# Performance work log

Measured on AMD Instinct MI355X. Metric: run time of the kernel, lower is better.

## Reference

```python
import jax, jax.numpy as jnp
import numpy as np

N_POINTS = 1 << 20
N_LEVELS = 16
F_PER_LVL = 2
LOG2_T = 19
T = 1 << LOG2_T
BASE_RES = 16
PER_LEVEL_SCALE = float(np.exp2(np.log2(2048.0 / 16.0) / (N_LEVELS - 1)))
# 8 trilinear corner offsets [8,3]
OFFSETS = np.stack(np.meshgrid(*([np.array([0, 1])] * 3), indexing='ij'), axis=-1).reshape(8, 3)
PRIMES = np.array([1, 2654435761, 805459861], dtype=np.uint32)  # tcnn spatial hash primes


def _level_params(l):
    # tcnn: grid_scale = 2^(l*log2(s)) * base - 1 ; resolution = ceil(scale)+1
    scale = np.exp2(l * np.log2(PER_LEVEL_SCALE)) * BASE_RES - 1.0
    res = int(np.ceil(scale)) + 1
    return float(scale), res


def hash_encode(x, table):
    """x: [N,3] in [0,1]; table: [L,T,F]. Returns [N, L*F]."""
    offs = jnp.asarray(OFFSETS)                     # [8,3] int32
    primes = jnp.asarray(PRIMES)                    # [3] uint32
    feats = []
    for l in range(N_LEVELS):
        scale, res = _level_params(l)
        pos = x * scale + 0.5                       # [N,3]
        pos_grid = jnp.floor(pos)
        w = pos - pos_grid                          # [N,3] interp weights
        c0 = pos_grid.astype(jnp.int32)             # [N,3]
        corners = c0[None, :, :] + offs[:, None, :]  # [8,N,3]
        if res ** 3 <= T:
            # dense indexing for coarse levels (fits in hashmap)
            cc = jnp.clip(corners, 0, res - 1)
            idx = cc[..., 0] + cc[..., 1] * res + cc[..., 2] * (res * res)
        else:
            cu = corners.astype(jnp.uint32)
            h = (cu[..., 0] * primes[0]) ^ (cu[..., 1] * primes[1]) ^ (cu[..., 2] * primes[2])
            idx = (h & jnp.uint32(T - 1)).astype(jnp.int32)
        f = table[l][idx]                           # [8,N,F] gather
        # trilinear weights: prod over dims of (w if corner bit else 1-w)
        wc = jnp.prod(jnp.where(offs[:, None, :] == 1, w[None], 1.0 - w[None]), axis=-1)  # [8,N]
        feats.append(jnp.sum(wc[..., None] * f, axis=0))  # [N,F]
    return jnp.concatenate(feats, axis=-1)          # [N, 32]


def _softplus10(z):
    return jax.nn.softplus(10.0 * z) / 10.0


def setup_inputs() -> dict:
    key = jax.random.key(0)
    k = jax.random.split(key, 6)
    x = jax.random.uniform(k[0], (N_POINTS, 3), dtype=jnp.float32)
    table = jax.random.normal(k[1], (N_LEVELS, T, F_PER_LVL), dtype=jnp.float32) * 1e-2
    w1 = jax.random.normal(k[2], (64, 32), dtype=jnp.float32) * 0.1
    w2 = jax.random.normal(k[3], (64, 64), dtype=jnp.float32) * 0.1
    w3 = jax.random.normal(k[4], (64, 64), dtype=jnp.float32) * 0.1
    w4 = jax.random.normal(k[5], (1, 64), dtype=jnp.float32) * 0.1
    return {"x": x, "table": table, "w1": w1, "w2": w2, "w3": w3, "w4": w4}


def reference(x, table, w1, w2, w3, w4):
    enc = hash_encode(x, table)                     # [N,32]
    h = _softplus10(enc @ w1.T)
    h = _softplus10(h @ w2.T)
    h = _softplus10(h @ w3.T)
    sdf = h @ w4.T                                  # [N,1]
    return sdf
```

## Files before the change

### kernel.cpp

```cpp
#include <hip/hip_runtime.h>
#include <cmath>

#define T_SIZE (1u << 19)
#define CB 512
#define NBLK 512
#define RCAP 3584

typedef _Float16 h8 __attribute__((ext_vector_type(8)));
typedef _Float16 h4 __attribute__((ext_vector_type(4)));
typedef _Float16 h2 __attribute__((ext_vector_type(2)));
typedef float f4 __attribute__((ext_vector_type(4)));

struct Levels {
    float scale[16];
    int   res[16];
    unsigned dense_mask;
};

__device__ __forceinline__ float softplus10(float z) {
    float e = __builtin_amdgcn_exp2f(fminf(z * 14.426950408889634f, 126.0f));
    return __builtin_amdgcn_logf(1.0f + e) * 0.069314718055994531f;
}

__device__ __forceinline__ unsigned spread3(unsigned v) {
    v &= 1023u;
    v = (v | (v << 16)) & 0x030000FFu;
    v = (v | (v << 8))  & 0x0300F00Fu;
    v = (v | (v << 4))  & 0x030C30C3u;
    v = (v | (v << 2))  & 0x09249249u;
    return v;
}

__device__ __forceinline__ unsigned morton_key(float px, float py, float pz) {
    unsigned qx = (unsigned)fminf(fmaxf(px, 0.f) * 32.f, 31.f);
    unsigned qy = (unsigned)fminf(fmaxf(py, 0.f) * 32.f, 31.f);
    unsigned qz = (unsigned)fminf(fmaxf(pz, 0.f) * 32.f, 31.f);
    return (spread3(qx) << 2) | (spread3(qy) << 1) | spread3(qz);
}

__global__ __launch_bounds__(256) void convert_kernel(
    const float2* __restrict__ t, h2* __restrict__ o, int total4,
    const float* __restrict__ w1, const float* __restrict__ w2,
    const float* __restrict__ w3, _Float16* __restrict__ wh,
    const float* __restrict__ xs, unsigned short* __restrict__ M, int N)
{
    const int histStart = (total4 + 10240 + 255) >> 8;
    if ((int)blockIdx.x >= histStart) {
        __shared__ unsigned h[CB];
        const int blk = blockIdx.x - histStart;
        for (int t2 = threadIdx.x; t2 < CB; t2 += 256) h[t2] = 0u;
        __syncthreads();
        const int s = blk * 2048;
#pragma unroll
        for (int j = 0; j < 8; ++j) {
            int i = s + threadIdx.x + j * 256;
            unsigned k = morton_key(xs[3 * i], xs[3 * i + 1], xs[3 * i + 2]) >> 6;
            atomicAdd(&h[k], 1u);
        }
        __syncthreads();
        for (int t2 = threadIdx.x; t2 < CB; t2 += 256)
            M[t2 * NBLK + blk] = (unsigned short)h[t2];
        return;
    }
    int i = blockIdx.x * 256 + threadIdx.x;
    if (i < total4) {
        const float2* src = t + (size_t)i * 4;
        h8 r;
#pragma unroll
        for (int j = 0; j < 4; ++j) {
            float2 v = src[j];
            r[2 * j]     = (_Float16)v.x;
            r[2 * j + 1] = (_Float16)v.y;
        }
        *(h8*)(o + (size_t)i * 4) = r;
    } else {
        int k = i - total4;
        if (k < 10240) {
            float v = (k < 2048) ? w1[k] : (k < 6144) ? w2[k - 2048] : w3[k - 6144];
            wh[k] = (_Float16)v;
        }
    }
}

__global__ __launch_bounds__(1024) void scan_kernel(
    const unsigned short* __restrict__ M, unsigned* __restrict__ Ms)
{
    __shared__ unsigned tmp[1024];
    const int t = threadIdx.x;
    const int PERS = (CB * NBLK) / 1024;
    unsigned s = 0;
    for (int j = 0; j < PERS; ++j) s += M[t * PERS + j];
    tmp[t] = s;
    __syncthreads();
    for (int d = 1; d < 1024; d <<= 1) {
        unsigned v = (t >= d) ? tmp[t - d] : 0u;
        __syncthreads();
        tmp[t] += v;
        __syncthreads();
    }
    unsigned run = (t > 0) ? tmp[t - 1] : 0u;
    for (int j = 0; j < PERS; ++j) {
        unsigned v = M[t * PERS + j];
        Ms[t * PERS + j] = run;
        run += v;
    }
}

__global__ __launch_bounds__(256) void cscatter_kernel(
    const float* __restrict__ xs, const unsigned* __restrict__ Ms,
    float4* __restrict__ sx4, int N)
{
    __shared__ float4  pts[2048];
    __shared__ unsigned gp[2048];
    __shared__ unsigned lh[CB];
    __shared__ unsigned lbase[CB];
    __shared__ unsigned tmp[256];
    const int tid = threadIdx.x;
    const int blk = blockIdx.x;
    for (int t2 = tid; t2 < CB; t2 += 256) lh[t2] = 0u;
    __syncthreads();
    const int s = blk * 2048;
    float4  myp[8];
    unsigned myk[8];
#pragma unroll
    for (int j = 0; j < 8; ++j) {
        int i = s + tid + j * 256;
        float px = xs[3 * i], py = xs[3 * i + 1], pz = xs[3 * i + 2];
        myp[j] = make_float4(px, py, pz, __uint_as_float((unsigned)i));
        myk[j] = morton_key(px, py, pz) >> 6;
        atomicAdd(&lh[myk[j]], 1u);
    }
    __syncthreads();
    unsigned a0 = lh[2 * tid], a1 = lh[2 * tid + 1];
    tmp[tid] = a0 + a1;
    __syncthreads();
    for (int d = 1; d < 256; d <<= 1) {
        unsigned v = (tid >= d) ? tmp[tid - d] : 0u;
        __syncthreads();
        tmp[tid] += v;
        __syncthreads();
    }
    unsigned eb = (tid > 0) ? tmp[tid - 1] : 0u;
    lbase[2 * tid] = eb;
    lbase[2 * tid + 1] = eb + a0;
    __syncthreads();
    lh[2 * tid] = 0u; lh[2 * tid + 1] = 0u;
    __syncthreads();
#pragma unroll
    for (int j = 0; j < 8; ++j) {
        unsigned k = myk[j];
        unsigned r = atomicAdd(&lh[k], 1u);
        unsigned slot = lbase[k] + r;
        pts[slot] = myp[j];
        gp[slot] = Ms[k * NBLK + blk] + r;
    }
    __syncthreads();
    for (int j = tid; j < 2048; j += 256)
        sx4[gp[j]] = pts[j];
}

__global__ __launch_bounds__(256) void refine_kernel(
    float4* __restrict__ sx4, const unsigned* __restrict__ Ms, int N)
{
    __shared__ float4 pts[RCAP];
    __shared__ unsigned h[64], base[64];
    const int b = blockIdx.x;
    const unsigned s = Ms[b * NBLK];
    const unsigned e = (b == CB - 1) ? (unsigned)N : Ms[(b + 1) * NBLK];
    const unsigned cnt = e - s;
    if (cnt > RCAP) return;
    if (threadIdx.x < 64) h[threadIdx.x] = 0u;
    __syncthreads();
    for (unsigned i = threadIdx.x; i < cnt; i += 256) {
        float4 q = sx4[s + i];
        pts[i] = q;
        unsigned k = morton_key(q.x, q.y, q.z) & 63u;
        atomicAdd(&h[k], 1u);
    }
    __syncthreads();
    if (threadIdx.x == 0) {
        unsigned a = 0;
        for (int j = 0; j < 64; ++j) { base[j] = a; a += h[j]; }
    }
    __syncthreads();
    if (threadIdx.x < 64) h[threadIdx.x] = 0u;
    __syncthreads();
    for (unsigned i = threadIdx.x; i < cnt; i += 256) {
        float4 q = pts[i];
        unsigned k = morton_key(q.x, q.y, q.z) & 63u;
        unsigned r = base[k] + atomicAdd(&h[k], 1u);
        sx4[s + r] = q;
    }
}

__device__ __forceinline__ void gather_pair(
    const h2* __restrict__ tl, unsigned i0, unsigned i1,
    float2& v0, float2& v1)
{
    unsigned e0, e1;
    if ((i0 ^ i1) == 1u) {
        uint2 both = *(const uint2*)(tl + (i0 & ~1u));
        e0 = (i0 & 1u) ? both.y : both.x;
        e1 = (i0 & 1u) ? both.x : both.y;
    } else {
        e0 = *(const unsigned*)(tl + i0);
        e1 = *(const unsigned*)(tl + i1);
    }
    h2 c0 = __builtin_bit_cast(h2, e0);
    h2 c1 = __builtin_bit_cast(h2, e1);
    v0 = make_float2((float)c0[0], (float)c0[1]);
    v1 = make_float2((float)c1[0], (float)c1[1]);
}

__device__ __forceinline__ h2 encode_point(
    float px, float py, float pz, float s, int res, bool dense,
    const h2* __restrict__ tl)
{
    float fx = px * s + 0.5f, fy = py * s + 0.5f, fz = pz * s + 0.5f;
    float gx = floorf(fx), gy = floorf(fy), gz = floorf(fz);
    float wx = fx - gx, wy = fy - gy, wz = fz - gz;
    int cx = (int)gx, cy = (int)gy, cz = (int)gz;

    float2 vx0[4], vx1[4];
    if (dense) {
        int r1 = res - 1;
        int x0 = min(cx, r1), x1 = min(cx + 1, r1);
        int y0 = min(cy, r1), y1 = min(cy + 1, r1);
        int z0 = min(cz, r1), z1 = min(cz + 1, r1);
        int rr = res * res;
        int bases[4] = {y0 * res + z0 * rr, y0 * res + z1 * rr,
                        y1 * res + z0 * rr, y1 * res + z1 * rr};
#pragma unroll
        for (int j = 0; j < 4; ++j)
            gather_pair(tl, (unsigned)(x0 + bases[j]), (unsigned)(x1 + bases[j]),
                        vx0[j], vx1[j]);
    } else {
        unsigned hy0 = (unsigned)cy * 2654435761u, hy1 = (unsigned)(cy + 1) * 2654435761u;
        unsigned hz0 = (unsigned)cz * 805459861u,  hz1 = (unsigned)(cz + 1) * 805459861u;
        unsigned Y[4] = {hy0 ^ hz0, hy0 ^ hz1, hy1 ^ hz0, hy1 ^ hz1};
        const unsigned M = T_SIZE - 1;
#pragma unroll
        for (int j = 0; j < 4; ++j)
            gather_pair(tl, ((unsigned)cx ^ Y[j]) & M,
                        ((unsigned)(cx + 1) ^ Y[j]) & M, vx0[j], vx1[j]);
    }

    float wx0 = 1.f - wx, wy0 = 1.f - wy, wz0 = 1.f - wz;
    float wyz[4] = {wy0 * wz0, wy0 * wz, wy * wz0, wy * wz};
    float f0 = 0.f, f1 = 0.f;
#pragma unroll
    for (int j = 0; j < 4; ++j) {
        float w0 = wx0 * wyz[j], w1 = wx * wyz[j];
        f0 += w0 * vx0[j].x + w1 * vx1[j].x;
        f1 += w0 * vx0[j].y + w1 * vx1[j].y;
    }
    h2 r; r[0] = (_Float16)f0; r[1] = (_Float16)f1;
    return r;
}

__global__ __launch_bounds__(256) void encode_kernel(
    const float* __restrict__ xs, const h2* __restrict__ table,
    h2* __restrict__ enc2, Levels lv, int lbase, int N)
{
    __shared__ float sx[768];
    const int i0 = blockIdx.x * 256;
    for (int t = threadIdx.x; t < 768; t += 256) sx[t] = xs[(size_t)i0 * 3 + t];
    __syncthreads();

    const int l = lbase + blockIdx.y;
    const int i = i0 + threadIdx.x;
    if (i >= N) return;
    h2 r = encode_point(sx[threadIdx.x * 3], sx[threadIdx.x * 3 + 1],
                        sx[threadIdx.x * 3 + 2], lv.scale[l], lv.res[l],
                        (lv.dense_mask >> l) & 1u, table + (size_t)l * T_SIZE);
    enc2[(size_t)l * N + i] = r;
}

__global__ __launch_bounds__(256) void encode_kernel_sorted(
    const float4* __restrict__ xs4, const h2* __restrict__ table,
    h2* __restrict__ enc2, Levels lv, int lbase, int N)
{
    const int i = blockIdx.x * 256 + threadIdx.x;
    if (i >= N) return;
    const int l = lbase + blockIdx.y;
    float4 q = xs4[i];
    h2 r = encode_point(q.x, q.y, q.z, lv.scale[l], lv.res[l],
                        (lv.dense_mask >> l) & 1u, table + (size_t)l * T_SIZE);
    enc2[(size_t)l * N + i] = r;
}

template <typename WT>
__device__ __forceinline__ h8 load_frag8(const WT* p) {
    if constexpr (sizeof(WT) == 2) {
        return *(const h8*)p;
    } else {
        h8 r;
#pragma unroll
        for (int j = 0; j < 8; ++j) r[j] = (_Float16)p[j];
        return r;
    }
}

template <typename WT, bool LOCAL, bool SORTED>
__global__ __launch_bounds__(256, 3) void fused_kernel(
    const float* __restrict__ xs, const float4* __restrict__ xs4,
    const h2* __restrict__ table16, const h2* __restrict__ enc2,
    const WT* __restrict__ w1, const WT* __restrict__ w2,
    const WT* __restrict__ w3, const float* __restrict__ w4,
    float* __restrict__ out, Levels lv, int N)
{
    constexpr int AR = 72;
    __shared__ __align__(16) char smem[4 * 9216];
    __shared__ float sx[768];

    const int tid  = threadIdx.x;
    const int wave = tid >> 6;
    const int lane = tid & 63;
    const int lrow = lane & 15;
    const int quad = lane >> 4;
    const int base = blockIdx.x * 256;
    char* wmem = smem + wave * 9216;
    const f4 zero = {0.f, 0.f, 0.f, 0.f};

    float px, py, pz;
    unsigned oi = 0;
    if constexpr (SORTED) {
        float4 q = xs4[base + tid];
        px = q.x; py = q.y; pz = q.z;
        oi = __float_as_uint(q.w);
    } else {
        for (int t = tid; t < 768; t += 256) sx[t] = xs[(size_t)base * 3 + t];
        __syncthreads();
        px = sx[tid * 3]; py = sx[tid * 3 + 1]; pz = sx[tid * 3 + 2];
    }
    const int p = tid & 63;

    if (LOCAL) {
#pragma unroll
        for (int l = 5; l < 15; ++l) {
            h2 v = enc2[(size_t)l * N + base + tid];
            *(h2*)(wmem + ((l >> 2) << 10) + (p << 4) + ((l & 3) << 2)) = v;
        }
        const int LMAP[6] = {0, 1, 2, 3, 4, 15};
#pragma unroll 2
        for (int s6 = 0; s6 < 6; ++s6) {
            const int l = LMAP[s6];
            h2 v = encode_point(px, py, pz, lv.scale[l], lv.res[l],
                                (lv.dense_mask >> l) & 1u,
                                table16 + (size_t)l * T_SIZE);
            *(h2*)(wmem + ((l >> 2) << 10) + (p << 4) + ((l & 3) << 2)) = v;
        }
    } else {
#pragma unroll
        for (int l = 0; l < 16; ++l) {
            h2 v = enc2[(size_t)l * N + base + tid];
            *(h2*)(wmem + ((l >> 2) << 10) + (p << 4) + ((l & 3) << 2)) = v;
        }
    }

    asm volatile("" ::: "memory");

    h8 aW1[4];
#pragma unroll
    for (int tm = 0; tm < 4; ++tm)
        aW1[tm] = load_frag8(w1 + (tm * 16 + lrow) * 32 + quad * 8);
    h8 aW2[4][2], aW3[4][2];
#pragma unroll
    for (int tm = 0; tm < 4; ++tm)
#pragma unroll
        for (int km = 0; km < 2; ++km) {
            aW2[tm][km] = load_frag8(w2 + (tm * 16 + lrow) * 64 + km * 32 + quad * 8);
            aW3[tm][km] = load_frag8(w3 + (tm * 16 + lrow) * 64 + km * 32 + quad * 8);
        }
    h4 w4q[4];
#pragma unroll
    for (int tm = 0; tm < 4; ++tm)
#pragma unroll
        for (int r = 0; r < 4; ++r) w4q[tm][r] = (_Float16)w4[tm * 16 + quad * 4 + r];

    h8 bin[4];
#pragma unroll
    for (int t = 0; t < 4; ++t)
        bin[t] = *(const h8*)(wmem + (quad << 10) + ((t * 16 + lrow) << 4));

    _Float16* wAct = (_Float16*)wmem;

#pragma unroll
    for (int t = 0; t < 4; ++t) {
        const int arow = (t * 16 + lrow) * AR;
#pragma unroll
        for (int tm = 0; tm < 4; ++tm) {
            f4 acc = __builtin_amdgcn_mfma_f32_16x16x32_f16(aW1[tm], bin[t], zero, 0, 0, 0);
            h4 pk;
#pragma unroll
            for (int r = 0; r < 4; ++r) pk[r] = (_Float16)softplus10(acc[r]);
            *(h4*)&wAct[arow + tm * 16 + quad * 4] = pk;
        }
    }

#pragma unroll
    for (int t = 0; t < 4; ++t) {
        const int arow = (t * 16 + lrow) * AR;
        h8 b0 = *(const h8*)&wAct[arow + quad * 8];
        h8 b1 = *(const h8*)&wAct[arow + 32 + quad * 8];
        f4 accs[4];
#pragma unroll
        for (int tm = 0; tm < 4; ++tm) {
            f4 acc = __builtin_amdgcn_mfma_f32_16x16x32_f16(aW2[tm][0], b0, zero, 0, 0, 0);
            acc     = __builtin_amdgcn_mfma_f32_16x16x32_f16(aW2[tm][1], b1, acc,  0, 0, 0);
            accs[tm] = acc;
        }
#pragma unroll
        for (int tm = 0; tm < 4; ++tm) {
            h4 pk;
#pragma unroll
            for (int r = 0; r < 4; ++r) pk[r] = (_Float16)softplus10(accs[tm][r]);
            *(h4*)&wAct[arow + tm * 16 + quad * 4] = pk;
        }
    }

#pragma unroll
    for (int t = 0; t < 4; ++t) {
        const int arow = (t * 16 + lrow) * AR;
        h8 b0 = *(const h8*)&wAct[arow + quad * 8];
        h8 b1 = *(const h8*)&wAct[arow + 32 + quad * 8];
        float sum = 0.f;
#pragma unroll
        for (int tm = 0; tm < 4; ++tm) {
            f4 acc = __builtin_amdgcn_mfma_f32_16x16x32_f16(aW3[tm][0], b0, zero, 0, 0, 0);
            acc     = __builtin_amdgcn_mfma_f32_16x16x32_f16(aW3[tm][1], b1, acc,  0, 0, 0);
#pragma unroll
            for (int r = 0; r < 4; ++r)
                sum += (float)w4q[tm][r] * softplus10(acc[r]);
        }
        sum += __shfl_xor(sum, 16, 64);
        sum += __shfl_xor(sum, 32, 64);
        if constexpr (SORTED) {
            unsigned t_oi = __shfl(oi, t * 16 + lrow, 64);
            if (quad == 0) out[t_oi] = sum;
        } else {
            if (quad == 0)
                out[base + wave * 64 + t * 16 + lrow] = sum;
        }
    }
}

__global__ __launch_bounds__(256) void encode_kernel_f32(
    const float* __restrict__ xs, const float2* __restrict__ table,
    h2* __restrict__ enc2, Levels lv, int N)
{
    const int i = blockIdx.x * 256 + threadIdx.x;
    const int l = blockIdx.y;
    if (i >= N) return;
    float px = xs[3 * i], py = xs[3 * i + 1], pz = xs[3 * i + 2];
    float s = lv.scale[l];
    int res = lv.res[l];
    float fx = px * s + 0.5f, fy = py * s + 0.5f, fz = pz * s + 0.5f;
    float gx = floorf(fx), gy = floorf(fy), gz = floorf(fz);
    float wx = fx - gx, wy = fy - gy, wz = fz - gz;
    int cx = (int)gx, cy = (int)gy, cz = (int)gz;
    unsigned idx[8];
    if ((lv.dense_mask >> l) & 1u) {
        int r1 = res - 1;
        int x0 = min(cx, r1), x1 = min(cx + 1, r1);
        int y0 = min(cy, r1), y1 = min(cy + 1, r1);
        int z0 = min(cz, r1), z1 = min(cz + 1, r1);
        int rr = res * res;
        idx[0] = x0 + y0 * res + z0 * rr; idx[1] = x0 + y0 * res + z1 * rr;
        idx[2] = x0 + y1 * res + z0 * rr; idx[3] = x0 + y1 * res + z1 * rr;
        idx[4] = x1 + y0 * res + z0 * rr; idx[5] = x1 + y0 * res + z1 * rr;
        idx[6] = x1 + y1 * res + z0 * rr; idx[7] = x1 + y1 * res + z1 * rr;
    } else {
        unsigned hx0 = (unsigned)cx, hx1 = (unsigned)(cx + 1);
        unsigned hy0 = (unsigned)cy * 2654435761u, hy1 = (unsigned)(cy + 1) * 2654435761u;
        unsigned hz0 = (unsigned)cz * 805459861u,  hz1 = (unsigned)(cz + 1) * 805459861u;
        idx[0] = (hx0^hy0^hz0) & (T_SIZE-1); idx[1] = (hx0^hy0^hz1) & (T_SIZE-1);
        idx[2] = (hx0^hy1^hz0) & (T_SIZE-1); idx[3] = (hx0^hy1^hz1) & (T_SIZE-1);
        idx[4] = (hx1^hy0^hz0) & (T_SIZE-1); idx[5] = (hx1^hy0^hz1) & (T_SIZE-1);
        idx[6] = (hx1^hy1^hz0) & (T_SIZE-1); idx[7] = (hx1^hy1^hz1) & (T_SIZE-1);
    }
    const float2* tl = table + (size_t)l * T_SIZE;
    float wx0 = 1.f - wx, wy0 = 1.f - wy, wz0 = 1.f - wz;
    float wcs[8] = {wx0*wy0*wz0, wx0*wy0*wz, wx0*wy*wz0, wx0*wy*wz,
                    wx*wy0*wz0,  wx*wy0*wz,  wx*wy*wz0,  wx*wy*wz};
    float f0 = 0.f, f1 = 0.f;
#pragma unroll
    for (int c = 0; c < 8; ++c) {
        float2 v = tl[idx[c]];
        f0 += wcs[c] * v.x; f1 += wcs[c] * v.y;
    }
    h2 r; r[0] = (_Float16)f0; r[1] = (_Float16)f1;
    enc2[(size_t)l * N + i] = r;
}

extern "C" void kernel_launch(void* const* d_in, const int* in_sizes, int n_in,
                              void* d_out, int out_size, void* d_ws, size_t ws_size,
                              hipStream_t stream) {
    const float* x     = (const float*)d_in[0];
    const float* table = (const float*)d_in[1];
    const float* w1    = (const float*)d_in[2];
    const float* w2    = (const float*)d_in[3];
    const float* w3    = (const float*)d_in[4];
    const float* w4    = (const float*)d_in[5];
    float* out = (float*)d_out;
    const int N = in_sizes[0] / 3;

    Levels lv;
    lv.dense_mask = 0;
    const double pls = exp2(log2(2048.0 / 16.0) / 15.0);
    const double lg  = log2(pls);
    for (int l = 0; l < 16; ++l) {
        double sc = exp2((double)l * lg) * 16.0 - 1.0;
        int res = (int)ceil(sc) + 1;
        lv.scale[l] = (float)sc;
        lv.res[l]   = res;
        if ((long long)res * res * res <= (long long)T_SIZE) lv.dense_mask |= (1u << l);
    }

    const size_t encBytes   = (size_t)16 * N * 4;
    const size_t tableBytes = (size_t)16 * T_SIZE * 4;
    const size_t whBytes    = 32768;
    const size_t sx4Bytes   = (size_t)N * 16;
    h2* enc2 = (h2*)d_ws;

    const int ptBlocks = (N + 255) / 256;

    if (ws_size >= encBytes + tableBytes + whBytes + sx4Bytes
        && N == NBLK * 2048) {
        h2* table16    = (h2*)((char*)d_ws + encBytes);
        _Float16* wh   = (_Float16*)((char*)d_ws + encBytes + tableBytes);
        float4* sx4    = (float4*)((char*)d_ws + encBytes + tableBytes + whBytes);
        unsigned short* M = (unsigned short*)d_ws;
        unsigned* Ms      = (unsigned*)((char*)d_ws + 1024 * 1024);

        const int total4 = 16 * T_SIZE / 4;
        const int convBlocks = (total4 + 10240 + 255) / 256;
        hipLaunchKernelGGL(convert_kernel, dim3(convBlocks + NBLK), dim3(256), 0,
                           stream, (const float2*)table, table16, total4,
                           w1, w2, w3, wh, x, M, N);
        hipLaunchKernelGGL(scan_kernel, dim3(1), dim3(1024), 0, stream, M, Ms);
        hipLaunchKernelGGL(cscatter_kernel, dim3(NBLK), dim3(256), 0, stream,
                           x, Ms, sx4, N);
        hipLaunchKernelGGL(refine_kernel, dim3(CB), dim3(256), 0, stream,
                           sx4, Ms, N);

        hipLaunchKernelGGL(encode_kernel_sorted, dim3(ptBlocks, 10), dim3(256), 0, stream,
                           (const float4*)sx4, (const h2*)table16, enc2, lv, 5, N);
        hipLaunchKernelGGL((fused_kernel<_Float16, true, true>), dim3(ptBlocks), dim3(256),
                           0, stream, x, (const float4*)sx4, (const h2*)table16,
                           (const h2*)enc2, wh, wh + 2048, wh + 6144, w4, out, lv, N);
    } else if (ws_size >= encBytes + tableBytes + whBytes) {
        h2* table16 = (h2*)((char*)d_ws + encBytes);
        _Float16* wh = (_Float16*)((char*)d_ws + encBytes + tableBytes);
        const int total4 = 16 * T_SIZE / 4;
        const int convBlocks = (total4 + 10240 + 255) / 256;
        hipLaunchKernelGGL(convert_kernel, dim3(convBlocks), dim3(256), 0, stream,
                           (const float2*)table, table16, total4, w1, w2, w3, wh,
                           x, (unsigned short*)nullptr, N);
        hipLaunchKernelGGL(encode_kernel, dim3(ptBlocks, 10), dim3(256), 0, stream,
                           x, (const h2*)table16, enc2, lv, 5, N);
        hipLaunchKernelGGL((fused_kernel<_Float16, true, false>), dim3(ptBlocks), dim3(256),
                           0, stream, x, (const float4*)nullptr, (const h2*)table16,
                           (const h2*)enc2, wh, wh + 2048, wh + 6144, w4, out, lv, N);
    } else {
        hipLaunchKernelGGL(encode_kernel_f32, dim3(ptBlocks, 16), dim3(256), 0, stream,
                           x, (const float2*)table, enc2, lv, N);
        hipLaunchKernelGGL((fused_kernel<float, false, false>), dim3(ptBlocks), dim3(256),
                           0, stream, x, (const float4*)nullptr, (const h2*)nullptr,
                           (const h2*)enc2, w1, w2, w3, w4, out, lv, N);
    }
}
```

Measured before the change: 481.3 us.

## Widen table gathers to 16-byte loads and process two points per thread

The corner gather now loads an aligned 16-byte group of four fp16 feature pairs, so the x-neighbour is taken from the same load whenever both fall in that group. The sorted encode kernel runs two points per thread: it computes all indices first, issues every gather, then interpolates, giving more loads in flight per thread. The scan kernel also reads its histogram with 16-byte vector loads. This adds register pressure and makes each gather wider than before, and the sorted encode kernel drops its bounds check, relying on N being a multiple of 512.

Measured after the change: 475.2 us. About the same (-1.3%).

```diff
diff --git a/kernel.cpp b/kernel.cpp
--- a/kernel.cpp
+++ b/kernel.cpp
@@ -88,8 +88,14 @@
     __shared__ unsigned tmp[1024];
     const int t = threadIdx.x;
     const int PERS = (CB * NBLK) / 1024;
+    const uint4* mv = (const uint4*)(M + t * PERS);
     unsigned s = 0;
-    for (int j = 0; j < PERS; ++j) s += M[t * PERS + j];
+#pragma unroll 4
+    for (int j = 0; j < PERS / 8; ++j) {
+        uint4 v = mv[j];
+        s += (v.x & 0xFFFFu) + (v.x >> 16) + (v.y & 0xFFFFu) + (v.y >> 16)
+           + (v.z & 0xFFFFu) + (v.z >> 16) + (v.w & 0xFFFFu) + (v.w >> 16);
+    }
     tmp[t] = s;
     __syncthreads();
     for (int d = 1; d < 1024; d <<= 1) {
@@ -197,13 +203,20 @@
     const h2* __restrict__ tl, unsigned i0, unsigned i1,
     float2& v0, float2& v1)
 {
-    unsigned e0, e1;
-    if ((i0 ^ i1) == 1u) {
-        uint2 both = *(const uint2*)(tl + (i0 & ~1u));
-        e0 = (i0 & 1u) ? both.y : both.x;
-        e1 = (i0 & 1u) ? both.x : both.y;
-    } else {
-        e0 = *(const unsigned*)(tl + i0);
+    unsigned g = i0 & ~3u;
+    union { h8 v; uint4 u; } cv;
+    cv.v = *(const h8*)(tl + g);
+    unsigned p0 = i0 & 3u;
+    unsigned a01 = (p0 & 1u) ? cv.u.y : cv.u.x;
+    unsigned a23 = (p0 & 1u) ? cv.u.w : cv.u.z;
+    unsigned e0  = (p0 & 2u) ? a23 : a01;
+    unsigned e1;
+    if ((i1 & ~3u) == g) {
+        unsigned p1 = i1 & 3u;
+        unsigned b01 = (p1 & 1u) ? cv.u.y : cv.u.x;
+        unsigned b23 = (p1 & 1u) ? cv.u.w : cv.u.z;
+        e1 = (p1 & 2u) ? b23 : b01;
+    } else {
         e1 = *(const unsigned*)(tl + i1);
     }
     h2 c0 = __builtin_bit_cast(h2, e0);
@@ -258,6 +271,79 @@
     return r;
 }
 
+struct PLCtx {
+    unsigned g[4], p0[4], i1[4], sg[4];
+    float wx, wy, wz;
+};
+
+__device__ __forceinline__ void prep_point(
+    float px, float py, float pz, float s, int res, bool dense, PLCtx& c)
+{
+    float fx = px * s + 0.5f, fy = py * s + 0.5f, fz = pz * s + 0.5f;
+    float gx = floorf(fx), gy = floorf(fy), gz = floorf(fz);
+    c.wx = fx - gx; c.wy = fy - gy; c.wz = fz - gz;
+    int cx = (int)gx, cy = (int)gy, cz = (int)gz;
+    unsigned i0[4], i1[4];
+    if (dense) {
+        int r1 = res - 1;
+        int x0 = min(cx, r1), x1 = min(cx + 1, r1);
+        int y0 = min(cy, r1), y1 = min(cy + 1, r1);
+        int z0 = min(cz, r1), z1 = min(cz + 1, r1);
+        int rr = res * res;
+        int bases[4] = {y0 * res + z0 * rr, y0 * res + z1 * rr,
+                        y1 * res + z0 * rr, y1 * res + z1 * rr};
+#pragma unroll
+        for (int j = 0; j < 4; ++j) {
+            i0[j] = (unsigned)(x0 + bases[j]);
+            i1[j] = (unsigned)(x1 + bases[j]);
+        }
+    } else {
+        unsigned hy0 = (unsigned)cy * 2654435761u, hy1 = (unsigned)(cy + 1) * 2654435761u;
+        unsigned hz0 = (unsigned)cz * 805459861u,  hz1 = (unsigned)(cz + 1) * 805459861u;
+        unsigned Y[4] = {hy0 ^ hz0, hy0 ^ hz1, hy1 ^ hz0, hy1 ^ hz1};
+        const unsigned M = T_SIZE - 1;
+#pragma unroll
+        for (int j = 0; j < 4; ++j) {
+            i0[j] = ((unsigned)cx ^ Y[j]) & M;
+            i1[j] = ((unsigned)(cx + 1) ^ Y[j]) & M;
+        }
+    }
+#pragma unroll
+    for (int j = 0; j < 4; ++j) {
+        c.g[j]  = i0[j] & ~3u;
+        c.p0[j] = i0[j] & 3u;
+        c.i1[j] = i1[j];
+        c.sg[j] = ((i1[j] & ~3u) == c.g[j]) ? 1u : 0u;
+    }
+}
+
+__device__ __forceinline__ h2 finish_point(
+    const uint4 cv[4], const unsigned e1x[4], const PLCtx& c)
+{
+    float wx0 = 1.f - c.wx, wy0 = 1.f - c.wy, wz0 = 1.f - c.wz;
+    float wyz[4] = {wy0 * wz0, wy0 * c.wz, c.wy * wz0, c.wy * c.wz};
+    float f0 = 0.f, f1 = 0.f;
+#pragma unroll
+    for (int j = 0; j < 4; ++j) {
+        unsigned p0 = c.p0[j];
+        unsigned a01 = (p0 & 1u) ? cv[j].y : cv[j].x;
+        unsigned a23 = (p0 & 1u) ? cv[j].w : cv[j].z;
+        unsigned e0  = (p0 & 2u) ? a23 : a01;
+        unsigned p1 = c.i1[j] & 3u;
+        unsigned b01 = (p1 & 1u) ? cv[j].y : cv[j].x;
+        unsigned b23 = (p1 & 1u) ? cv[j].w : cv[j].z;
+        unsigned eg  = (p1 & 2u) ? b23 : b01;
+        unsigned e1  = c.sg[j] ? eg : e1x[j];
+        h2 c0 = __builtin_bit_cast(h2, e0);
+        h2 c1 = __builtin_bit_cast(h2, e1);
+        float w0 = wx0 * wyz[j], w1 = c.wx * wyz[j];
+        f0 += w0 * (float)c0[0] + w1 * (float)c1[0];
+        f1 += w0 * (float)c0[1] + w1 * (float)c1[1];
+    }
+    h2 r; r[0] = (_Float16)f0; r[1] = (_Float16)f1;
+    return r;
+}
+
 __global__ __launch_bounds__(256) void encode_kernel(
     const float* __restrict__ xs, const h2* __restrict__ table,
     h2* __restrict__ enc2, Levels lv, int lbase, int N)
@@ -280,13 +366,34 @@
     const float4* __restrict__ xs4, const h2* __restrict__ table,
     h2* __restrict__ enc2, Levels lv, int lbase, int N)
 {
-    const int i = blockIdx.x * 256 + threadIdx.x;
-    if (i >= N) return;
+    const int i = blockIdx.x * 512 + threadIdx.x;
     const int l = lbase + blockIdx.y;
-    float4 q = xs4[i];
-    h2 r = encode_point(q.x, q.y, q.z, lv.scale[l], lv.res[l],
-                        (lv.dense_mask >> l) & 1u, table + (size_t)l * T_SIZE);
-    enc2[(size_t)l * N + i] = r;
+    const h2* tl = table + (size_t)l * T_SIZE;
+    const float s = lv.scale[l];
+    const int res = lv.res[l];
+    const bool dense = (lv.dense_mask >> l) & 1u;
+
+    float4 qa = xs4[i];
+    float4 qb = xs4[i + 256];
+    PLCtx ca, cb;
+    prep_point(qa.x, qa.y, qa.z, s, res, dense, ca);
+    prep_point(qb.x, qb.y, qb.z, s, res, dense, cb);
+
+    uint4 cva[4], cvb[4];
+    unsigned ea[4], eb[4];
+#pragma unroll
+    for (int j = 0; j < 4; ++j) cva[j] = *(const uint4*)(tl + ca.g[j]);
+#pragma unroll
+    for (int j = 0; j < 4; ++j) cvb[j] = *(const uint4*)(tl + cb.g[j]);
+#pragma unroll
+    for (int j = 0; j < 4; ++j)
+        ea[j] = ca.sg[j] ? 0u : *(const unsigned*)(tl + ca.i1[j]);
+#pragma unroll
+    for (int j = 0; j < 4; ++j)
+        eb[j] = cb.sg[j] ? 0u : *(const unsigned*)(tl + cb.i1[j]);
+
+    enc2[(size_t)l * N + i]       = finish_point(cva, ea, ca);
+    enc2[(size_t)l * N + i + 256] = finish_point(cvb, eb, cb);
 }
 
 template <typename WT>
@@ -544,8 +651,9 @@
         hipLaunchKernelGGL(refine_kernel, dim3(CB), dim3(256), 0, stream,
                            sx4, Ms, N);
 
-        hipLaunchKernelGGL(encode_kernel_sorted, dim3(ptBlocks, 10), dim3(256), 0, stream,
-                           (const float4*)sx4, (const h2*)table16, enc2, lv, 5, N);
+        hipLaunchKernelGGL(encode_kernel_sorted, dim3(ptBlocks / 2, 10), dim3(256),
+                           0, stream, (const float4*)sx4, (const h2*)table16,
+                           enc2, lv, 5, N);
         hipLaunchKernelGGL((fused_kernel<_Float16, true, true>), dim3(ptBlocks), dim3(256),
                            0, stream, x, (const float4*)sx4, (const h2*)table16,
                            (const h2*)enc2, wh, wh + 2048, wh + 6144, w4, out, lv, N);
```
